# Kernel optimization log

Hardware: AMD Instinct MI355X
Metric: run time of the kernel (lower is better)

The kernel has to match this reference:

```python
import jax, jax.numpy as jnp
import numpy as np

N_HEAD = 16


def setup_inputs() -> dict:
    key = jax.random.key(0)
    ks = jax.random.split(key, 5)
    B, L, C = 2, 2048, 1024
    s = 0.02
    return {
        "x": jax.random.normal(ks[0], (B, L, C), dtype=jnp.float32),
        "attn_mask": jnp.ones((B, L), dtype=jnp.int64),
        "Wq": jax.random.normal(ks[1], (C, C), dtype=jnp.float32) * s,
        "Wk": jax.random.normal(ks[2], (C, C), dtype=jnp.float32) * s,
        "Wv": jax.random.normal(ks[3], (C, C), dtype=jnp.float32) * s,
        "Wp": jax.random.normal(ks[4], (C, C), dtype=jnp.float32) * s,
    }


def reference(x, attn_mask, Wq, Wk, Wv, Wp):
    B, L, C = x.shape
    H = N_HEAD
    D = C // H
    # nn.Linear(bias=False): y = x @ W.T with W of shape (out, in)
    q = (x @ Wq.T).reshape(B, L, H, D).transpose(0, 2, 1, 3)  # (B,H,L,D)
    k = (x @ Wk.T).reshape(B, L, H, D).transpose(0, 2, 1, 3)
    v = (x @ Wv.T).reshape(B, L, H, D).transpose(0, 2, 1, 3)
    att = jnp.einsum("bhqd,bhkd->bhqk", q, k) / jnp.sqrt(jnp.asarray(D, x.dtype))
    causal = jnp.tril(jnp.ones((L, L), dtype=bool))  # (L,L)
    tok = (attn_mask != 0)[:, None, None, :]  # (B,1,1,L) key-side padding mask
    mask = causal[None, None, :, :] & tok
    att = jnp.where(mask, att, -jnp.inf)
    att = jax.nn.softmax(att, axis=-1)
    # dropout p=0.0 (eval): identity
    y = jnp.einsum("bhqk,bhkd->bhqd", att, v)
    y = y.transpose(0, 2, 1, 3).reshape(B, L, C)
    return y @ Wp.T
```

## Files before the change

kernel.cpp:

```cpp
#include <hip/hip_runtime.h>
#include <hip/hip_bf16.h>
#include <cstdint>

typedef _Float16 f16;
typedef _Float16 f16x4 __attribute__((ext_vector_type(4)));
typedef _Float16 f16x8 __attribute__((ext_vector_type(8)));
typedef float f32x4 __attribute__((ext_vector_type(4)));

#define LNEG (-1e30f)
#define EXP2(x) __builtin_amdgcn_exp2f(x)

__device__ __forceinline__ f32x4 mfma16(f16x8 a, f16x8 b, f32x4 c){
    return __builtin_amdgcn_mfma_f32_16x16x32_f16(a, b, c, 0, 0, 0);
}

__global__ __launch_bounds__(256) void cvt5(
    const float* __restrict__ x,  const float* __restrict__ wq,
    const float* __restrict__ wk, const float* __restrict__ wv,
    const float* __restrict__ wp, f16* __restrict__ dst, int nx8)
{
    int i = blockIdx.x * blockDim.x + threadIdx.x;
    const float* src; int off;
    if (i < nx8){ src = x; off = i; }
    else {
        int j = i - nx8;
        int s = j >> 17;
        off = j & 131071;
        src = (s == 0) ? wq : (s == 1) ? wk : (s == 2) ? wv : wp;
    }
    const float4* p = (const float4*)src + (size_t)off * 2;
    float4 v0 = p[0], v1 = p[1];
    f16x8 o = { (f16)v0.x, (f16)v0.y, (f16)v0.z, (f16)v0.w,
                (f16)v1.x, (f16)v1.y, (f16)v1.z, (f16)v1.w };
    *(f16x8*)&dst[(size_t)i * 8] = o;
}

template<typename OutT>
__global__ __launch_bounds__(256) void gemm_xwt(
    const f16* __restrict__ A, const f16* __restrict__ W0, size_t wstride,
    OutT* __restrict__ out0, size_t ostride, f16* __restrict__ vtout,
    int M, int N, int K)
{
    const int tid  = threadIdx.x;
    const int lane = tid & 63;
    const int w    = tid >> 6;
    const int wr   = w >> 1, wc = w & 1;
    const int m0   = blockIdx.y * 128;
    const int n0   = blockIdx.x * 128;
    const f16* Wz  = W0 + wstride * blockIdx.z;
    OutT* out      = out0 + ostride * blockIdx.z;

    __shared__ f16 At[2][128 * 64];
    __shared__ f16 Bt[2][128 * 64];

    f32x4 acc[4][4] = {};
    f16x8 avr[4], bvr[4];

    int srow[4], scolb[4], sswz[4];
    #pragma unroll
    for (int j = 0; j < 4; ++j){
        int off  = (j * 256 + tid) * 16;
        srow[j]  = off >> 7;
        scolb[j] = off & 127;
        sswz[j]  = srow[j] * 128 + (scolb[j] ^ ((srow[j] & 7) << 4));
    }

    #pragma unroll
    for (int j = 0; j < 4; ++j){
        avr[j] = *(const f16x8*)&A [(size_t)(m0 + srow[j]) * K + (scolb[j] >> 1)];
        bvr[j] = *(const f16x8*)&Wz[(size_t)(n0 + srow[j]) * K + (scolb[j] >> 1)];
    }
    #pragma unroll
    for (int j = 0; j < 4; ++j){
        *(f16x8*)((char*)At[0] + sswz[j]) = avr[j];
        *(f16x8*)((char*)Bt[0] + sswz[j]) = bvr[j];
    }
    __syncthreads();

    const int NT = K >> 6;
    for (int t = 0; t < NT; ++t){
        const int cur = t & 1;
        const bool pre = (t + 1 < NT);
        if (pre){
            const int k0 = (t + 1) << 6;
            #pragma unroll
            for (int j = 0; j < 4; ++j){
                avr[j] = *(const f16x8*)&A [(size_t)(m0 + srow[j]) * K + k0 + (scolb[j] >> 1)];
                bvr[j] = *(const f16x8*)&Wz[(size_t)(n0 + srow[j]) * K + k0 + (scolb[j] >> 1)];
            }
        }
        #pragma unroll
        for (int kk = 0; kk < 2; ++kk){
            f16x8 af[4], bf[4];
            #pragma unroll
            for (int mf = 0; mf < 4; ++mf){
                int row = wr * 64 + mf * 16 + (lane & 15);
                int cb  = (kk * 64 + 16 * (lane >> 4)) ^ ((row & 7) << 4);
                af[mf] = *(const f16x8*)((const char*)At[cur] + row * 128 + cb);
            }
            #pragma unroll
            for (int nf = 0; nf < 4; ++nf){
                int row = wc * 64 + nf * 16 + (lane & 15);
                int cb  = (kk * 64 + 16 * (lane >> 4)) ^ ((row & 7) << 4);
                bf[nf] = *(const f16x8*)((const char*)Bt[cur] + row * 128 + cb);
            }
            #pragma unroll
            for (int mf = 0; mf < 4; ++mf)
                #pragma unroll
                for (int nf = 0; nf < 4; ++nf)
                    acc[mf][nf] = mfma16(af[mf], bf[nf], acc[mf][nf]);
        }
        if (pre){
            const int nb = cur ^ 1;
            #pragma unroll
            for (int j = 0; j < 4; ++j){
                *(f16x8*)((char*)At[nb] + sswz[j]) = avr[j];
                *(f16x8*)((char*)Bt[nb] + sswz[j]) = bvr[j];
            }
        }
        __syncthreads();
    }

    if (vtout != nullptr && blockIdx.z == 2){
        #pragma unroll
        for (int mf = 0; mf < 4; ++mf)
            #pragma unroll
            for (int nf = 0; nf < 4; ++nf){
                int row = m0 + wr * 64 + mf * 16 + 4 * (lane >> 4);
                int col = n0 + wc * 64 + nf * 16 + (lane & 15);
                int bb = row >> 11, ll = row & 2047;
                int bh = bb * 16 + (col >> 6), dd = col & 63;
                f16x4 o = { (f16)acc[mf][nf][0], (f16)acc[mf][nf][1],
                            (f16)acc[mf][nf][2], (f16)acc[mf][nf][3] };
                *(f16x4*)&vtout[((size_t)(bh * 64 + dd)) * 2048 + ll] = o;
            }
    } else {
        #pragma unroll
        for (int mf = 0; mf < 4; ++mf)
            #pragma unroll
            for (int nf = 0; nf < 4; ++nf)
                #pragma unroll
                for (int r = 0; r < 4; ++r){
                    int row = m0 + wr * 64 + mf * 16 + 4 * (lane >> 4) + r;
                    int col = n0 + wc * 64 + nf * 16 + (lane & 15);
                    out[(size_t)row * N + col] = (OutT)acc[mf][nf][r];
                }
    }
}

__global__ __launch_bounds__(256, 4) void attn_fused(
    const f16* __restrict__ q, const f16* __restrict__ k,
    const f16* __restrict__ vt, const int* __restrict__ amask,
    f16* __restrict__ y)
{
    const int tid  = threadIdx.x;
    const int lane = tid & 63;
    const int w    = tid >> 6;
    const int g    = lane >> 4;
    const int qq   = lane & 15;

    const int lin = blockIdx.x;
    const int bh  = ((lin & 7) << 2) | ((lin >> 3) & 3);
    const int qtv = (lin >> 5) & 31;
    const int q5  = (qtv & 7) | ((qtv & 16) >> 1);
    const int qt  = (qtv & 8) ? (31 - q5) : q5;
    const int b = bh >> 4, h = bh & 15;
    const int q0w = qt * 64 + w * 16;
    const int nkt = qt + 1;

    __shared__ char sK[2][64 * 128];
    __shared__ char sV[2][64 * 128];
    __shared__ char sP[4][16 * 128];

    const int srow = (tid * 2) >> 3;
    const int sc8a = (tid * 2) & 7, sc8b = sc8a + 1;
    const int swka = (sc8a * 16) ^ ((srow & 7) << 4);
    const int swkb = (sc8b * 16) ^ ((srow & 7) << 4);
    const f16* kbase  = k  + ((size_t)b * 2048) * 1024 + h * 64;
    const f16* vtbase = vt + (size_t)bh * 64 * 2048;

    const f16 qscale = (f16)(0.125f * 1.44269504088896f);
    f16x8 aq[2];
    #pragma unroll
    for (int f = 0; f < 2; ++f){
        aq[f] = *(const f16x8*)&q[((size_t)(b * 2048 + q0w + qq)) * 1024 + h * 64 + f * 32 + 8 * g];
        #pragma unroll
        for (int j = 0; j < 8; ++j) aq[f][j] *= qscale;
    }

    f32x4 acc_o[4] = {};
    float m_ln = LNEG, l_ln = 0.f;

    char* pbase = sP[w] + qq * 128;
    const int swp = (qq & 7) << 4;

    {
        f16x8 ka  = *(const f16x8*)(kbase  + (size_t)srow * 1024 + sc8a * 8);
        f16x8 kb2 = *(const f16x8*)(kbase  + (size_t)srow * 1024 + sc8b * 8);
        f16x8 va  = *(const f16x8*)(vtbase + (size_t)srow * 2048 + sc8a * 8);
        f16x8 vb  = *(const f16x8*)(vtbase + (size_t)srow * 2048 + sc8b * 8);
        *(f16x8*)(sK[0] + srow * 128 + swka) = ka;
        *(f16x8*)(sK[0] + srow * 128 + swkb) = kb2;
        *(f16x8*)(sV[0] + srow * 128 + swka) = va;
        *(f16x8*)(sV[0] + srow * 128 + swkb) = vb;
    }
    __syncthreads();

    for (int kt = 0; kt < nkt; ++kt){
        const int cur = kt & 1;
        const int k0 = kt * 64;
        const bool pre = (kt + 1 < nkt);

        f16x8 ka, kb2, va, vb;
        if (pre){
            const int nk0 = k0 + 64;
            ka  = *(const f16x8*)(kbase  + (size_t)(nk0 + srow) * 1024 + sc8a * 8);
            kb2 = *(const f16x8*)(kbase  + (size_t)(nk0 + srow) * 1024 + sc8b * 8);
            va  = *(const f16x8*)(vtbase + (size_t)srow * 2048 + nk0 + sc8a * 8);
            vb  = *(const f16x8*)(vtbase + (size_t)srow * 2048 + nk0 + sc8b * 8);
        }

        unsigned long long tokbits = __ballot(amask[b * 2048 + k0 + lane] != 0);
        const bool tokall = (tokbits == ~0ull);

        f32x4 acc_s[4] = {};
        #pragma unroll
        for (int kf = 0; kf < 4; ++kf){
            const int keyl = kf * 16 + qq;
            const char* kr = sK[cur] + keyl * 128;
            const int sw = (keyl & 7) << 4;
            #pragma unroll
            for (int f = 0; f < 2; ++f){
                f16x8 ak = *(const f16x8*)(kr + ((f * 64 + 16 * g) ^ sw));
                acc_s[kf] = mfma16(ak, aq[f], acc_s[kf]);
            }
        }

        const bool fullt = (k0 + 63 <= q0w) && tokall;
        float sv[16];
        #pragma unroll
        for (int kf = 0; kf < 4; ++kf)
            #pragma unroll
            for (int r = 0; r < 4; ++r){
                float s = acc_s[kf][r];
                if (!fullt){
                    const int keyl = kf * 16 + 4 * g + r;
                    const bool ok = (k0 + keyl <= q0w + qq) && ((tokbits >> keyl) & 1);
                    s = ok ? s : LNEG;
                }
                sv[kf * 4 + r] = s;
            }

        float tmax = sv[0];
        #pragma unroll
        for (int i = 1; i < 16; ++i) tmax = fmaxf(tmax, sv[i]);
        tmax = fmaxf(tmax, __shfl_xor(tmax, 16));
        tmax = fmaxf(tmax, __shfl_xor(tmax, 32));
        const bool skip = __all(tmax <= m_ln + 8.f);
        float alpha = 1.f;
        if (!skip){
            const float newm = fmaxf(m_ln, tmax);
            alpha = EXP2(m_ln - newm);
            m_ln = newm;
        }
        #pragma unroll
        for (int i = 0; i < 16; ++i) sv[i] = EXP2(sv[i] - m_ln);
        if (!skip){
            #pragma unroll
            for (int r = 0; r < 4; ++r){
                const float ar = __shfl(alpha, 4 * g + r);
                #pragma unroll
                for (int nf = 0; nf < 4; ++nf) acc_o[nf][r] *= ar;
            }
        }

        #pragma unroll
        for (int kf = 0; kf < 4; ++kf){
            f16x4 pk = { (f16)sv[kf*4+0], (f16)sv[kf*4+1], (f16)sv[kf*4+2], (f16)sv[kf*4+3] };
            *(f16x4*)(pbase + ((kf * 32 + 8 * g) ^ swp)) = pk;
        }
        __builtin_amdgcn_wave_barrier();

        #pragma unroll
        for (int f = 0; f < 2; ++f){
            f16x8 ap = *(const f16x8*)(pbase + ((f * 64 + 16 * g) ^ swp));
            #pragma unroll
            for (int nf = 0; nf < 4; ++nf){
                const int d = nf * 16 + qq;
                f16x8 bv = *(const f16x8*)(sV[cur] + d * 128 + ((f * 64 + 16 * g) ^ ((d & 7) << 4)));
                acc_o[nf] = mfma16(ap, bv, acc_o[nf]);
            }
        }

        {
            float rs = 0.f;
            #pragma unroll
            for (int i = 0; i < 16; ++i) rs += sv[i];
            rs += __shfl_xor(rs, 16);
            rs += __shfl_xor(rs, 32);
            l_ln = l_ln * alpha + rs;
        }
        __builtin_amdgcn_wave_barrier();

        if (pre){
            const int nb = cur ^ 1;
            *(f16x8*)(sK[nb] + srow * 128 + swka) = ka;
            *(f16x8*)(sK[nb] + srow * 128 + swkb) = kb2;
            *(f16x8*)(sV[nb] + srow * 128 + swka) = va;
            *(f16x8*)(sV[nb] + srow * 128 + swkb) = vb;
        }
        __syncthreads();
    }

    const float invl = 1.f / l_ln;
    #pragma unroll
    for (int r = 0; r < 4; ++r){
        const float ir = __shfl(invl, 4 * g + r);
        const int row = q0w + 4 * g + r;
        #pragma unroll
        for (int nf = 0; nf < 4; ++nf)
            y[((size_t)(b * 2048 + row)) * 1024 + h * 64 + nf * 16 + qq] = (f16)(acc_o[nf][r] * ir);
    }
}

extern "C" void kernel_launch(void* const* d_in, const int* in_sizes, int n_in,
                              void* d_out, int out_size, void* d_ws, size_t ws_size,
                              hipStream_t stream){
    const float* x  = (const float*)d_in[0];
    const int*   am = (const int*)d_in[1];
    const float* Wq = (const float*)d_in[2];
    const float* Wk = (const float*)d_in[3];
    const float* Wv = (const float*)d_in[4];
    const float* Wp = (const float*)d_in[5];
    float* out = (float*)d_out;

    char* ws = (char*)d_ws;
    const size_t XE = (size_t)4096 * 1024;
    const size_t WE = (size_t)1024 * 1024;

    f16* x16 = (f16*)(ws);
    f16* w16 = (f16*)(ws + XE * 2);
    f16* qkv = (f16*)(ws + XE * 2 + WE * 8);
    f16* vt  = (f16*)(ws + XE * 2 + WE * 8 + XE * 6);
    f16* y16 = (f16*)(ws + XE * 2 + WE * 8 + XE * 8);

    cvt5<<<4096, 256, 0, stream>>>(x, Wq, Wk, Wv, Wp, x16, (int)(XE / 8));

    gemm_xwt<f16><<<dim3(8, 32, 3), 256, 0, stream>>>(x16, w16, WE, qkv, XE, vt, 4096, 1024, 1024);

    attn_fused<<<dim3(1024), 256, 0, stream>>>(qkv, qkv + XE, vt, am, y16);

    gemm_xwt<float><<<dim3(8, 32, 1), 256, 0, stream>>>(y16, w16 + 3 * WE, 0, out, 0, nullptr, 4096, 1024, 1024);
}
```

Before: 116.5 us.

## Process two 16-row query tiles per wave in attention to reuse K/V fragments

Each wave in the attention kernel now handles 32 query rows instead of 16, so a block covers 128 queries and the grid halves to 512 blocks. Every K and V fragment read from shared memory feeds two MFMAs, which halves LDS traffic and global K/V loads per query. The cost is double the accumulator and score registers, a lower occupancy hint (launch bounds 2), coarser causal load balancing, and fewer blocks to fill the GPU.

After: 131.7 us. 13.0% more time.

```diff
diff --git a/kernel.cpp b/kernel.cpp
--- a/kernel.cpp
+++ b/kernel.cpp
@@ -148,7 +148,7 @@
     }
 }
 
-__global__ __launch_bounds__(256, 4) void attn_fused(
+__global__ __launch_bounds__(256, 2) void attn_fused(
     const f16* __restrict__ q, const f16* __restrict__ k,
     const f16* __restrict__ vt, const int* __restrict__ amask,
     f16* __restrict__ y)
@@ -161,16 +161,15 @@
 
     const int lin = blockIdx.x;
     const int bh  = ((lin & 7) << 2) | ((lin >> 3) & 3);
-    const int qtv = (lin >> 5) & 31;
-    const int q5  = (qtv & 7) | ((qtv & 16) >> 1);
-    const int qt  = (qtv & 8) ? (31 - q5) : q5;
+    const int qtI = (lin >> 5) & 15;
+    const int qt  = (qtI < 8) ? qtI : 23 - qtI;
     const int b = bh >> 4, h = bh & 15;
-    const int q0w = qt * 64 + w * 16;
-    const int nkt = qt + 1;
+    const int q0w = qt * 128 + w * 32;
+    const int nkt = 2 * qt + 2;
 
     __shared__ char sK[2][64 * 128];
     __shared__ char sV[2][64 * 128];
-    __shared__ char sP[4][16 * 128];
+    __shared__ char sP[4][2][16 * 128];
 
     const int srow = (tid * 2) >> 3;
     const int sc8a = (tid * 2) & 7, sc8b = sc8a + 1;
@@ -180,18 +179,18 @@
     const f16* vtbase = vt + (size_t)bh * 64 * 2048;
 
     const f16 qscale = (f16)(0.125f * 1.44269504088896f);
-    f16x8 aq[2];
-    #pragma unroll
-    for (int f = 0; f < 2; ++f){
-        aq[f] = *(const f16x8*)&q[((size_t)(b * 2048 + q0w + qq)) * 1024 + h * 64 + f * 32 + 8 * g];
-        #pragma unroll
-        for (int j = 0; j < 8; ++j) aq[f][j] *= qscale;
-    }
-
-    f32x4 acc_o[4] = {};
-    float m_ln = LNEG, l_ln = 0.f;
-
-    char* pbase = sP[w] + qq * 128;
+    f16x8 aq[2][2];
+    #pragma unroll
+    for (int p = 0; p < 2; ++p)
+        #pragma unroll
+        for (int f = 0; f < 2; ++f){
+            aq[p][f] = *(const f16x8*)&q[((size_t)(b * 2048 + q0w + 16 * p + qq)) * 1024 + h * 64 + f * 32 + 8 * g];
+            #pragma unroll
+            for (int j = 0; j < 8; ++j) aq[p][f][j] *= qscale;
+        }
+
+    f32x4 acc_o[2][4] = {};
+    float m_st[2] = { LNEG, LNEG }, l_st[2] = { 0.f, 0.f };
     const int swp = (qq & 7) << 4;
 
     {
@@ -223,7 +222,7 @@
         unsigned long long tokbits = __ballot(amask[b * 2048 + k0 + lane] != 0);
         const bool tokall = (tokbits == ~0ull);
 
-        f32x4 acc_s[4] = {};
+        f32x4 accS[2][4] = {};
         #pragma unroll
         for (int kf = 0; kf < 4; ++kf){
             const int keyl = kf * 16 + qq;
@@ -232,73 +231,76 @@
             #pragma unroll
             for (int f = 0; f < 2; ++f){
                 f16x8 ak = *(const f16x8*)(kr + ((f * 64 + 16 * g) ^ sw));
-                acc_s[kf] = mfma16(ak, aq[f], acc_s[kf]);
-            }
-        }
-
-        const bool fullt = (k0 + 63 <= q0w) && tokall;
-        float sv[16];
-        #pragma unroll
-        for (int kf = 0; kf < 4; ++kf)
-            #pragma unroll
-            for (int r = 0; r < 4; ++r){
-                float s = acc_s[kf][r];
-                if (!fullt){
-                    const int keyl = kf * 16 + 4 * g + r;
-                    const bool ok = (k0 + keyl <= q0w + qq) && ((tokbits >> keyl) & 1);
-                    s = ok ? s : LNEG;
+                accS[0][kf] = mfma16(ak, aq[0][f], accS[0][kf]);
+                accS[1][kf] = mfma16(ak, aq[1][f], accS[1][kf]);
+            }
+        }
+
+        #pragma unroll
+        for (int p = 0; p < 2; ++p){
+            const int q0p = q0w + 16 * p;
+            const bool fullt = (k0 + 63 <= q0p) && tokall;
+            float sv[16];
+            #pragma unroll
+            for (int kf = 0; kf < 4; ++kf)
+                #pragma unroll
+                for (int r = 0; r < 4; ++r){
+                    float s = accS[p][kf][r];
+                    if (!fullt){
+                        const int keyl = kf * 16 + 4 * g + r;
+                        const bool ok = (k0 + keyl <= q0p + qq) && ((tokbits >> keyl) & 1);
+                        s = ok ? s : LNEG;
+                    }
+                    sv[kf * 4 + r] = s;
                 }
-                sv[kf * 4 + r] = s;
-            }
-
-        float tmax = sv[0];
-        #pragma unroll
-        for (int i = 1; i < 16; ++i) tmax = fmaxf(tmax, sv[i]);
-        tmax = fmaxf(tmax, __shfl_xor(tmax, 16));
-        tmax = fmaxf(tmax, __shfl_xor(tmax, 32));
-        const bool skip = __all(tmax <= m_ln + 8.f);
-        float alpha = 1.f;
-        if (!skip){
-            const float newm = fmaxf(m_ln, tmax);
-            alpha = EXP2(m_ln - newm);
-            m_ln = newm;
-        }
-        #pragma unroll
-        for (int i = 0; i < 16; ++i) sv[i] = EXP2(sv[i] - m_ln);
-        if (!skip){
-            #pragma unroll
-            for (int r = 0; r < 4; ++r){
-                const float ar = __shfl(alpha, 4 * g + r);
+
+            float tmax = sv[0];
+            #pragma unroll
+            for (int i = 1; i < 16; ++i) tmax = fmaxf(tmax, sv[i]);
+            tmax = fmaxf(tmax, __shfl_xor(tmax, 16));
+            tmax = fmaxf(tmax, __shfl_xor(tmax, 32));
+            const bool skip = __all(tmax <= m_st[p] + 8.f);
+            float alpha = 1.f;
+            if (!skip){
+                const float newm = fmaxf(m_st[p], tmax);
+                alpha = EXP2(m_st[p] - newm);
+                m_st[p] = newm;
+            }
+            float rs = 0.f;
+            #pragma unroll
+            for (int i = 0; i < 16; ++i){ sv[i] = EXP2(sv[i] - m_st[p]); rs += sv[i]; }
+            rs += __shfl_xor(rs, 16);
+            rs += __shfl_xor(rs, 32);
+            l_st[p] = l_st[p] * alpha + rs;
+            if (!skip){
                 #pragma unroll
-                for (int nf = 0; nf < 4; ++nf) acc_o[nf][r] *= ar;
-            }
-        }
-
-        #pragma unroll
-        for (int kf = 0; kf < 4; ++kf){
-            f16x4 pk = { (f16)sv[kf*4+0], (f16)sv[kf*4+1], (f16)sv[kf*4+2], (f16)sv[kf*4+3] };
-            *(f16x4*)(pbase + ((kf * 32 + 8 * g) ^ swp)) = pk;
+                for (int r = 0; r < 4; ++r){
+                    const float ar = __shfl(alpha, 4 * g + r);
+                    #pragma unroll
+                    for (int nf = 0; nf < 4; ++nf) acc_o[p][nf][r] *= ar;
+                }
+            }
+
+            char* pbase = sP[w][p] + qq * 128;
+            #pragma unroll
+            for (int kf = 0; kf < 4; ++kf){
+                f16x4 pk = { (f16)sv[kf*4+0], (f16)sv[kf*4+1], (f16)sv[kf*4+2], (f16)sv[kf*4+3] };
+                *(f16x4*)(pbase + ((kf * 32 + 8 * g) ^ swp)) = pk;
+            }
         }
         __builtin_amdgcn_wave_barrier();
 
         #pragma unroll
         for (int f = 0; f < 2; ++f){
-            f16x8 ap = *(const f16x8*)(pbase + ((f * 64 + 16 * g) ^ swp));
+            f16x8 apA = *(const f16x8*)(sP[w][0] + qq * 128 + ((f * 64 + 16 * g) ^ swp));
+            f16x8 apB = *(const f16x8*)(sP[w][1] + qq * 128 + ((f * 64 + 16 * g) ^ swp));
             #pragma unroll
             for (int nf = 0; nf < 4; ++nf){
                 const int d = nf * 16 + qq;
                 f16x8 bv = *(const f16x8*)(sV[cur] + d * 128 + ((f * 64 + 16 * g) ^ ((d & 7) << 4)));
-                acc_o[nf] = mfma16(ap, bv, acc_o[nf]);
-            }
-        }
-
-        {
-            float rs = 0.f;
-            #pragma unroll
-            for (int i = 0; i < 16; ++i) rs += sv[i];
-            rs += __shfl_xor(rs, 16);
-            rs += __shfl_xor(rs, 32);
-            l_ln = l_ln * alpha + rs;
+                acc_o[0][nf] = mfma16(apA, bv, acc_o[0][nf]);
+                acc_o[1][nf] = mfma16(apB, bv, acc_o[1][nf]);
+            }
         }
         __builtin_amdgcn_wave_barrier();
 
@@ -312,14 +314,17 @@
         __syncthreads();
     }
 
-    const float invl = 1.f / l_ln;
-    #pragma unroll
-    for (int r = 0; r < 4; ++r){
-        const float ir = __shfl(invl, 4 * g + r);
-        const int row = q0w + 4 * g + r;
-        #pragma unroll
-        for (int nf = 0; nf < 4; ++nf)
-            y[((size_t)(b * 2048 + row)) * 1024 + h * 64 + nf * 16 + qq] = (f16)(acc_o[nf][r] * ir);
+    #pragma unroll
+    for (int p = 0; p < 2; ++p){
+        const float invl = 1.f / l_st[p];
+        #pragma unroll
+        for (int r = 0; r < 4; ++r){
+            const float ir = __shfl(invl, 4 * g + r);
+            const int row = q0w + 16 * p + 4 * g + r;
+            #pragma unroll
+            for (int nf = 0; nf < 4; ++nf)
+                y[((size_t)(b * 2048 + row)) * 1024 + h * 64 + nf * 16 + qq] = (f16)(acc_o[p][nf][r] * ir);
+        }
     }
 }
 
@@ -348,7 +353,7 @@
 
     gemm_xwt<f16><<<dim3(8, 32, 3), 256, 0, stream>>>(x16, w16, WE, qkv, XE, vt, 4096, 1024, 1024);
 
-    attn_fused<<<dim3(1024), 256, 0, stream>>>(qkv, qkv + XE, vt, am, y16);
+    attn_fused<<<dim3(512), 256, 0, stream>>>(qkv, qkv + XE, vt, am, y16);
 
     gemm_xwt<float><<<dim3(8, 32, 1), 256, 0, stream>>>(y16, w16 + 3 * WE, 0, out, 0, nullptr, 4096, 1024, 1024);
 }
```

## Split long causal query tiles across two blocks and merge partial softmax results

Applied to the files above, without the earlier changes.

Query tiles 20–31 now have their key range split in two (keys 0–15 and 16..qt). Each half runs as a separate block that writes unnormalized fp32 partial outputs plus running max and sum to workspace. A new merge kernel combines the two halves with log-sum-exp weighting. This caps per-block work at about 16 key tiles, which should shorten the critical path set by the longest causal blocks in a grid that fits in a single wave. It costs extra global traffic, an extra launch, and per-iteration __syncthreads in place of wave barriers, and the row-sum is now computed before the PV MFMAs.

Result: faster. 110.7 us (-5.0%).

```diff
diff --git a/kernel.cpp b/kernel.cpp
--- a/kernel.cpp
+++ b/kernel.cpp
@@ -151,7 +151,7 @@
 __global__ __launch_bounds__(256, 4) void attn_fused(
     const f16* __restrict__ q, const f16* __restrict__ k,
     const f16* __restrict__ vt, const int* __restrict__ amask,
-    f16* __restrict__ y)
+    f16* __restrict__ y, float* __restrict__ pO, float* __restrict__ pML)
 {
     const int tid  = threadIdx.x;
     const int lane = tid & 63;
@@ -160,13 +160,16 @@
     const int qq   = lane & 15;
 
     const int lin = blockIdx.x;
-    const int bh  = ((lin & 7) << 2) | ((lin >> 3) & 3);
-    const int qtv = (lin >> 5) & 31;
-    const int q5  = (qtv & 7) | ((qtv & 16) >> 1);
-    const int qt  = (qtv & 8) ? (31 - q5) : q5;
+    const int bh  = lin & 31;
+    const int grp = lin >> 5;
+    int qt, ktLo, ktHi, part; bool fin;
+    if (grp < 4)      { qt = 19 - grp;  ktLo = 0;  ktHi = qt + 1; fin = true;  part = 0; }
+    else if (grp < 16){ qt = 16 + grp;  ktLo = 0;  ktHi = 16;     fin = false; part = 0; }
+    else if (grp < 28){ qt = 47 - grp;  ktLo = 16; ktHi = qt + 1; fin = false; part = 1; }
+    else              { qt = 43 - grp;  ktLo = 0;  ktHi = qt + 1; fin = true;  part = 0; }
+
     const int b = bh >> 4, h = bh & 15;
     const int q0w = qt * 64 + w * 16;
-    const int nkt = qt + 1;
 
     __shared__ char sK[2][64 * 128];
     __shared__ char sV[2][64 * 128];
@@ -195,10 +198,11 @@
     const int swp = (qq & 7) << 4;
 
     {
-        f16x8 ka  = *(const f16x8*)(kbase  + (size_t)srow * 1024 + sc8a * 8);
-        f16x8 kb2 = *(const f16x8*)(kbase  + (size_t)srow * 1024 + sc8b * 8);
-        f16x8 va  = *(const f16x8*)(vtbase + (size_t)srow * 2048 + sc8a * 8);
-        f16x8 vb  = *(const f16x8*)(vtbase + (size_t)srow * 2048 + sc8b * 8);
+        const int k0p = ktLo * 64;
+        f16x8 ka  = *(const f16x8*)(kbase  + (size_t)(k0p + srow) * 1024 + sc8a * 8);
+        f16x8 kb2 = *(const f16x8*)(kbase  + (size_t)(k0p + srow) * 1024 + sc8b * 8);
+        f16x8 va  = *(const f16x8*)(vtbase + (size_t)srow * 2048 + k0p + sc8a * 8);
+        f16x8 vb  = *(const f16x8*)(vtbase + (size_t)srow * 2048 + k0p + sc8b * 8);
         *(f16x8*)(sK[0] + srow * 128 + swka) = ka;
         *(f16x8*)(sK[0] + srow * 128 + swkb) = kb2;
         *(f16x8*)(sV[0] + srow * 128 + swka) = va;
@@ -206,10 +210,10 @@
     }
     __syncthreads();
 
-    for (int kt = 0; kt < nkt; ++kt){
-        const int cur = kt & 1;
+    for (int kt = ktLo; kt < ktHi; ++kt){
+        const int cur = (kt - ktLo) & 1;
         const int k0 = kt * 64;
-        const bool pre = (kt + 1 < nkt);
+        const bool pre = (kt + 1 < ktHi);
 
         f16x8 ka, kb2, va, vb;
         if (pre){
@@ -263,8 +267,12 @@
             alpha = EXP2(m_ln - newm);
             m_ln = newm;
         }
-        #pragma unroll
-        for (int i = 0; i < 16; ++i) sv[i] = EXP2(sv[i] - m_ln);
+        float rs = 0.f;
+        #pragma unroll
+        for (int i = 0; i < 16; ++i){ sv[i] = EXP2(sv[i] - m_ln); rs += sv[i]; }
+        rs += __shfl_xor(rs, 16);
+        rs += __shfl_xor(rs, 32);
+        l_ln = l_ln * alpha + rs;
         if (!skip){
             #pragma unroll
             for (int r = 0; r < 4; ++r){
@@ -279,7 +287,7 @@
             f16x4 pk = { (f16)sv[kf*4+0], (f16)sv[kf*4+1], (f16)sv[kf*4+2], (f16)sv[kf*4+3] };
             *(f16x4*)(pbase + ((kf * 32 + 8 * g) ^ swp)) = pk;
         }
-        __builtin_amdgcn_wave_barrier();
+        __syncthreads();
 
         #pragma unroll
         for (int f = 0; f < 2; ++f){
@@ -291,16 +299,6 @@
                 acc_o[nf] = mfma16(ap, bv, acc_o[nf]);
             }
         }
-
-        {
-            float rs = 0.f;
-            #pragma unroll
-            for (int i = 0; i < 16; ++i) rs += sv[i];
-            rs += __shfl_xor(rs, 16);
-            rs += __shfl_xor(rs, 32);
-            l_ln = l_ln * alpha + rs;
-        }
-        __builtin_amdgcn_wave_barrier();
 
         if (pre){
             const int nb = cur ^ 1;
@@ -312,15 +310,71 @@
         __syncthreads();
     }
 
-    const float invl = 1.f / l_ln;
+    if (fin){
+        const float invl = 1.f / l_ln;
+        #pragma unroll
+        for (int r = 0; r < 4; ++r){
+            const float ir = __shfl(invl, 4 * g + r);
+            const int row = q0w + 4 * g + r;
+            #pragma unroll
+            for (int nf = 0; nf < 4; ++nf)
+                y[((size_t)(b * 2048 + row)) * 1024 + h * 64 + nf * 16 + qq] = (f16)(acc_o[nf][r] * ir);
+        }
+    } else {
+        const int qi = qt - 20;
+        const size_t base = (((size_t)part * 12 + qi) * 32 + bh) * 64;
+        #pragma unroll
+        for (int r = 0; r < 4; ++r){
+            const int row_local = w * 16 + 4 * g + r;
+            float* po = pO + (base + row_local) * 64;
+            #pragma unroll
+            for (int nf = 0; nf < 4; ++nf)
+                po[nf * 16 + qq] = acc_o[nf][r];
+        }
+        if (lane < 16){
+            const size_t mlb = (base + w * 16 + lane) * 2;
+            pML[mlb]     = m_ln;
+            pML[mlb + 1] = l_ln;
+        }
+    }
+}
+
+__global__ __launch_bounds__(256) void attn_merge(
+    const float* __restrict__ pO, const float* __restrict__ pML, f16* __restrict__ y)
+{
+    const int t = blockIdx.x * 256 + threadIdx.x;
+    const int dc = (t & 3) * 16;
+    const int rowg = t >> 2;
+    const int row = rowg & 63;
+    const int bh  = (rowg >> 6) & 31;
+    const int qi  = rowg >> 11;
+    const size_t rbase = ((size_t)qi * 32 + bh) * 64 + row;
+    const size_t PST = (size_t)12 * 32 * 64;
+
+    const float mA = pML[rbase * 2],         lA = pML[rbase * 2 + 1];
+    const float mB = pML[(PST + rbase) * 2], lB = pML[(PST + rbase) * 2 + 1];
+    const float m  = fmaxf(mA, mB);
+    const float wA = EXP2(mA - m), wB = EXP2(mB - m);
+    const float inv = 1.f / (wA * lA + wB * lB);
+
+    const float4* oA = (const float4*)(pO + rbase * 64 + dc);
+    const float4* oB = (const float4*)(pO + (PST * 64) + rbase * 64 + dc);
+    float ov[16];
     #pragma unroll
-    for (int r = 0; r < 4; ++r){
-        const float ir = __shfl(invl, 4 * g + r);
-        const int row = q0w + 4 * g + r;
-        #pragma unroll
-        for (int nf = 0; nf < 4; ++nf)
-            y[((size_t)(b * 2048 + row)) * 1024 + h * 64 + nf * 16 + qq] = (f16)(acc_o[nf][r] * ir);
-    }
+    for (int j = 0; j < 4; ++j){
+        float4 a = oA[j], bb4 = oB[j];
+        ov[j*4+0] = (wA * a.x + wB * bb4.x) * inv;
+        ov[j*4+1] = (wA * a.y + wB * bb4.y) * inv;
+        ov[j*4+2] = (wA * a.z + wB * bb4.z) * inv;
+        ov[j*4+3] = (wA * a.w + wB * bb4.w) * inv;
+    }
+    const int b = bh >> 4, h = bh & 15;
+    const int grow = (20 + qi) * 64 + row;
+    f16* yp = &y[((size_t)(b * 2048 + grow)) * 1024 + h * 64 + dc];
+    f16x8 o0 = { (f16)ov[0],(f16)ov[1],(f16)ov[2],(f16)ov[3],(f16)ov[4],(f16)ov[5],(f16)ov[6],(f16)ov[7] };
+    f16x8 o1 = { (f16)ov[8],(f16)ov[9],(f16)ov[10],(f16)ov[11],(f16)ov[12],(f16)ov[13],(f16)ov[14],(f16)ov[15] };
+    *(f16x8*)yp = o0;
+    *(f16x8*)(yp + 8) = o1;
 }
 
 extern "C" void kernel_launch(void* const* d_in, const int* in_sizes, int n_in,
@@ -343,12 +397,16 @@
     f16* qkv = (f16*)(ws + XE * 2 + WE * 8);
     f16* vt  = (f16*)(ws + XE * 2 + WE * 8 + XE * 6);
     f16* y16 = (f16*)(ws + XE * 2 + WE * 8 + XE * 8);
+    float* pO  = (float*)ws;
+    float* pML = (float*)(ws + (size_t)2*12*32*64*64*4);
 
     cvt5<<<4096, 256, 0, stream>>>(x, Wq, Wk, Wv, Wp, x16, (int)(XE / 8));
 
     gemm_xwt<f16><<<dim3(8, 32, 3), 256, 0, stream>>>(x16, w16, WE, qkv, XE, vt, 4096, 1024, 1024);
 
-    attn_fused<<<dim3(1024), 256, 0, stream>>>(qkv, qkv + XE, vt, am, y16);
+    attn_fused<<<dim3(1408), 256, 0, stream>>>(qkv, qkv + XE, vt, am, y16, pO, pML);
+
+    attn_merge<<<384, 256, 0, stream>>>(pO, pML, y16);
 
     gemm_xwt<float><<<dim3(8, 32, 1), 256, 0, stream>>>(y16, w16 + 3 * WE, 0, out, 0, nullptr, 4096, 1024, 1024);
 }
```
